# Performance work log

Hardware: AMD Instinct MI355X
Metric: run time of the kernel (lower is better)

The kernel has to match this reference:

```python
import jax, jax.numpy as jnp
import numpy as np

NUM_HEADS = 16


def rotate_half(x):
    x1 = x[..., ::2]
    x2 = x[..., 1::2]
    return jnp.concatenate((-x2, x1), axis=-1)


def rope_sin_cos(seq_len, head_dim, dtype):
    inv_freq = 1.0 / (10000.0 ** (jnp.arange(0, head_dim, 2, dtype=jnp.float32) / head_dim))
    t = jnp.arange(seq_len, dtype=jnp.float32)
    freqs = jnp.einsum('i,j->ij', t, inv_freq)          # [S, D/2]
    emb = jnp.concatenate((freqs, freqs), axis=-1)      # [S, D]
    return jnp.sin(emb).astype(dtype), jnp.cos(emb).astype(dtype)


def setup_inputs() -> dict:
    key = jax.random.key(0)
    B, S, E = 2, 2048, 2048
    ks = jax.random.split(key, 5)
    scale = 1.0 / np.sqrt(E)
    return {
        'x': jax.random.normal(ks[0], (B, S, E), dtype=jnp.float32),
        'mask': jnp.ones((B, S), dtype=jnp.int32),
        'Wq': jax.random.normal(ks[1], (E, E), dtype=jnp.float32) * scale,
        'bq': jnp.zeros((E,), dtype=jnp.float32),
        'Wk': jax.random.normal(ks[2], (E, E), dtype=jnp.float32) * scale,
        'bk': jnp.zeros((E,), dtype=jnp.float32),
        'Wv': jax.random.normal(ks[3], (E, E), dtype=jnp.float32) * scale,
        'bv': jnp.zeros((E,), dtype=jnp.float32),
        'Wo': jax.random.normal(ks[4], (E, E), dtype=jnp.float32) * scale,
        'bo': jnp.zeros((E,), dtype=jnp.float32),
    }


def reference(x, mask, Wq, bq, Wk, bk, Wv, bv, Wo, bo):
    B, S, E = x.shape
    H = NUM_HEADS
    D = E // H
    q = (x @ Wq + bq).reshape(B, S, H, D).transpose(0, 2, 1, 3)  # [B,H,S,D]
    k = (x @ Wk + bk).reshape(B, S, H, D).transpose(0, 2, 1, 3)
    v = (x @ Wv + bv).reshape(B, S, H, D).transpose(0, 2, 1, 3)

    sin, cos = rope_sin_cos(S, D, q.dtype)  # [S,D]
    sin = sin[None, None]                    # [1,1,S,D]
    cos = cos[None, None]
    q = q * cos + rotate_half(q) * sin
    k = k * cos + rotate_half(k) * sin

    scores = jnp.einsum('bhqd,bhkd->bhqk', q, k) / jnp.sqrt(jnp.asarray(D, q.dtype))
    scores = jnp.where(mask[:, None, None, :] == 0, -jnp.inf, scores)
    probs = jax.nn.softmax(scores, axis=-1)
    attn = jnp.einsum('bhqk,bhkd->bhqd', probs, v)       # [B,H,S,D]
    attn = attn.transpose(0, 2, 1, 3).reshape(B, S, E)
    return attn @ Wo + bo
```

## Files before the change

kernel.cpp:

```cpp
#include <hip/hip_runtime.h>
#include <hip/hip_bf16.h>
#include <cmath>

typedef unsigned short u16;
typedef unsigned int   u32;

using v4f    = __attribute__((ext_vector_type(4)))  float;
using f32x16 = __attribute__((ext_vector_type(16))) float;
using s8v    = __attribute__((ext_vector_type(8)))  short;
using u32x2  = __attribute__((ext_vector_type(2)))  unsigned int;

union Frag { uint4 u; s8v s; };

__device__ __forceinline__ u16 f2bf(float f){
  u32 u = __float_as_uint(f);
  u32 r = u + 0x7fffu + ((u >> 16) & 1u);
  return (u16)(r >> 16);
}
__device__ __forceinline__ float bf2f(u16 h){ return __uint_as_float(((u32)h) << 16); }

__device__ __forceinline__ u32 cvtpk(float a, float b){
  u32 r;
  asm("v_cvt_pk_bf16_f32 %0, %1, %2" : "=v"(r) : "v"(a), "v"(b));
  return r;
}

__device__ __forceinline__ void async16(const void* g, void* l){
  __builtin_amdgcn_global_load_lds((__attribute__((address_space(1))) void*)g,
                                   (__attribute__((address_space(3))) void*)l, 16, 0, 0);
}

__global__ __launch_bounds__(256) void prep_kernel(
    const float* __restrict__ x, u16* __restrict__ xb,
    const float* __restrict__ W0, const float* __restrict__ W1,
    const float* __restrict__ W2, const float* __restrict__ W3,
    u16* __restrict__ T0, u16* __restrict__ T1, u16* __restrict__ T2, u16* __restrict__ T3){
  __shared__ float tile[64][65];
  const int bid = blockIdx.x;
  if (bid < 8192){
    size_t i = ((size_t)bid * 256 + threadIdx.x) * 4;
    float4 v = *(const float4*)(x + i);
    uint2 o;
    o.x = (u32)f2bf(v.x) | ((u32)f2bf(v.y) << 16);
    o.y = (u32)f2bf(v.z) | ((u32)f2bf(v.w) << 16);
    *(uint2*)(xb + i) = o;
    return;
  }
  const int t4 = bid - 8192;
  const int z  = t4 >> 10;
  const float* W = (z==0)?W0:(z==1)?W1:(z==2)?W2:W3;
  u16*         T = (z==0)?T0:(z==1)?T1:(z==2)?T2:T3;
  const int k0 = ((t4 & 1023) >> 5)*64, n0 = (t4 & 31)*64;
  const int t  = threadIdx.x;
  const int rr = t >> 4, c4 = (t & 15) * 4;
  #pragma unroll
  for (int i=0;i<4;i++){
    int k = rr + i*16;
    float4 v = *(const float4*)(W + (size_t)(k0+k)*2048 + n0 + c4);
    tile[k][c4+0]=v.x; tile[k][c4+1]=v.y; tile[k][c4+2]=v.z; tile[k][c4+3]=v.w;
  }
  __syncthreads();
  #pragma unroll
  for (int i=0;i<4;i++){
    int n = rr + i*16;
    uint2 o;
    o.x = (u32)f2bf(tile[c4+0][n]) | ((u32)f2bf(tile[c4+1][n])<<16);
    o.y = (u32)f2bf(tile[c4+2][n]) | ((u32)f2bf(tile[c4+3][n])<<16);
    *(uint2*)(T + (size_t)(n0+n)*2048 + k0 + c4) = o;
  }
}

template<int MODE>
__device__ __forceinline__ void gemm_tile(const u16* __restrict__ A, const u16* __restrict__ BT,
                                          const float* __restrict__ bias, void* __restrict__ Cout,
                                          int m0, int n0, u16* sm){
  constexpr int K = 2048;
  u16* Asl = sm;
  u16* Bsl = sm + 8192;
  const int tid  = threadIdx.x;
  const int w    = tid >> 6;
  const int lane = tid & 63;
  const int r    = lane & 15, q = lane >> 4;
  const int wm   = (w >> 1) * 64, wn = (w & 1) * 64;

  v4f acc[4][4];
  #pragma unroll
  for (int i=0;i<4;i++)
    #pragma unroll
    for (int j=0;j<4;j++) acc[i][j] = (v4f)0.f;

  const int srow = w*32 + (lane>>3);
  const int sblk = (lane&7) ^ ((lane>>3)&7);
  const u16* Ag = A  + (size_t)(m0+srow)*K + sblk*8;
  const u16* Bg = BT + (size_t)(n0+srow)*K + sblk*8;
  u16* Als = Asl + (w*32)*64;
  u16* Bls = Bsl + (w*32)*64;

  for (int kk = 0; kk < K; kk += 64) {
    #pragma unroll
    for (int i=0;i<4;i++){
      async16(Ag + (size_t)i*8*K + kk, Als + i*512);
      async16(Bg + (size_t)i*8*K + kk, Bls + i*512);
    }
    __syncthreads();
    #pragma unroll
    for (int ks=0; ks<2; ++ks) {
      s8v af[4], bfr[4];
      #pragma unroll
      for (int i=0;i<4;i++){
        int rho = wm + i*16 + r;
        int p = (ks*4 + q) ^ (r&7);
        Frag t; t.u = *(const uint4*)(Asl + rho*64 + p*8); af[i] = t.s;
      }
      #pragma unroll
      for (int j=0;j<4;j++){
        int rho = wn + j*16 + r;
        int p = (ks*4 + q) ^ (r&7);
        Frag t; t.u = *(const uint4*)(Bsl + rho*64 + p*8); bfr[j] = t.s;
      }
      #pragma unroll
      for (int i=0;i<4;i++)
        #pragma unroll
        for (int j=0;j<4;j++)
          acc[i][j] = __builtin_amdgcn_mfma_f32_16x16x32_bf16(af[i], bfr[j], acc[i][j], 0, 0, 0);
    }
    __syncthreads();
  }

  float bv[4];
  #pragma unroll
  for (int j=0;j<4;j++) bv[j] = bias[n0 + wn + j*16 + r];

  if constexpr (MODE != 3){
    #pragma unroll
    for (int i=0;i<4;i++){
      #pragma unroll
      for (int j=0;j<4;j++){
        const int gn = n0 + wn + j*16 + r;
        #pragma unroll
        for (int rr2=0; rr2<4; ++rr2){
          const int gm = m0 + wm + i*16 + q*4 + rr2;
          float val = acc[i][j][rr2] + bv[j];
          if (MODE == 0) ((u16*)Cout)[(size_t)gm*2048 + gn] = f2bf(val);
          else           ((float*)Cout)[(size_t)gm*2048 + gn] = val;
        }
      }
    }
  } else {
    #pragma unroll
    for (int i=0;i<4;i++)
      #pragma unroll
      for (int j=0;j<4;j++){
        const int col = wn + j*16 + r;
        #pragma unroll
        for (int rr2=0; rr2<4; ++rr2)
          sm[(wm + i*16 + q*4 + rr2)*128 + col] = f2bf(acc[i][j][rr2] + bv[j]);
      }
    __syncthreads();
    const float invf = exp2f(-(float)lane * 0.20762050593045952f);
    for (int rr=0; rr<32; ++rr){
      const int row = w*32 + rr;
      const int s = (m0 + row) & 2047;
      float sn, cs;
      sincosf((float)s * invf, &sn, &cs);
      const u16* tr = sm + row*128;
      float x_j   = bf2f(tr[lane]);
      float x_j64 = bf2f(tr[64 + lane]);
      float x_2j  = bf2f(tr[2*lane]);
      float x_2j1 = bf2f(tr[2*lane + 1]);
      u16* gp = (u16*)Cout + (size_t)(m0 + row)*2048 + n0;
      gp[lane]      = f2bf(x_j  * cs - x_2j1 * sn);
      gp[64 + lane] = f2bf(x_j64 * cs + x_2j  * sn);
    }
  }
}

__global__ __launch_bounds__(256) void gemm_qkv_kernel(
    const u16* __restrict__ A,
    const u16* __restrict__ WqT, const u16* __restrict__ WkT, const u16* __restrict__ WvT,
    const float* __restrict__ bq, const float* __restrict__ bk, const float* __restrict__ bv,
    u16* __restrict__ Qb, u16* __restrict__ Kb, u16* __restrict__ Vb){
  __shared__ u16 sm[16384];
  const int bx = blockIdx.x, by = blockIdx.y;
  const int mat = bx >> 4;
  const u16*   BT   = (mat==0)?WqT:(mat==1)?WkT:WvT;
  const float* bias = (mat==0)?bq :(mat==1)?bk :bv;
  u16*         Cout = (mat==0)?Qb :(mat==1)?Kb :Vb;
  if (mat < 2) gemm_tile<3>(A, BT, bias, Cout, by*128, (bx & 15)*128, sm);
  else         gemm_tile<0>(A, BT, bias, Cout, by*128, (bx & 15)*128, sm);
}

__global__ __launch_bounds__(256) void gemm_wo_kernel(const u16* __restrict__ A,
                                                      const u16* __restrict__ WoT,
                                                      const float* __restrict__ bias,
                                                      float* __restrict__ out){
  __shared__ u16 sm[16384];
  gemm_tile<1>(A, WoT, bias, out, blockIdx.y*128, blockIdx.x*128, sm);
}

__global__ __launch_bounds__(256) void tv_kernel(const u16* __restrict__ V, u16* __restrict__ VT){
  __shared__ u16 t[64*72];
  const int tb = blockIdx.x;
  const int s0 = (tb & 31)*64;
  const int d0 = ((tb >> 5) & 1)*64;
  const int bh = tb >> 6;
  const int b = bh >> 4, h = bh & 15;
  const size_t obase = ((size_t)bh*128 + d0)*2048 + s0;
  const int tid = threadIdx.x;
  #pragma unroll
  for (int i=0;i<2;i++){
    int c = tid + i*256;
    int sl = c >> 3, dc = (c & 7) * 8;
    *(uint4*)(t + sl*72 + dc) =
      *(const uint4*)(V + ((size_t)(b*2048 + s0 + sl))*2048 + h*128 + d0 + dc);
  }
  __syncthreads();
  #pragma unroll
  for (int i=0;i<2;i++){
    int c = tid + i*256;
    int dl = c >> 3, sc4 = (c & 7) * 8;
    u16 tmp[8];
    #pragma unroll
    for (int j=0;j<8;j++) tmp[j] = t[(sc4+j)*72 + dl];
    *(uint4*)(VT + obase + (size_t)dl*2048 + sc4) = *(const uint4*)tmp;
  }
}

__global__ __launch_bounds__(256,2) void attn_kernel(const u16* __restrict__ Q,
                                                     const u16* __restrict__ K,
                                                     const u16* __restrict__ VT,
                                                     const int* __restrict__ mask,
                                                     u16* __restrict__ Out){
  constexpr int S = 2048;
  constexpr float SL2 = 0.08838834764831845f * 1.4426950408889634f;
  __shared__ u16 smem[32768];

  const int tid = threadIdx.x, w = tid >> 6, lane = tid & 63;
  const int qc = lane & 31;
  const int h  = lane >> 5;
  const int l7 = lane & 7;
  const int hh = blockIdx.y, b = blockIdx.z;
  const int q0 = blockIdx.x * 128;
  const size_t rowb = (size_t)b * 2048;
  const size_t bhD  = ((size_t)(b*16 + hh)) * 128;

  s8v qf[8];
  {
    const u16* qp = Q + (rowb + q0 + w*32 + qc)*2048 + hh*128 + h*8;
    #pragma unroll
    for (int t=0;t<8;t++){ Frag f; f.u = *(const uint4*)(qp + t*16); qf[t] = f.s; }
  }

  f32x16 accO[4];
  #pragma unroll
  for (int d=0; d<4; d++) accO[d] = (f32x16)0.f;
  float lsum = 0.f;

  const int sr4 = lane >> 4, sp16 = lane & 15;
  const int vr8 = lane >> 3, vp8 = lane & 7;

  auto stage = [&](u16* base, int key0){
    u16* Kd = base;
    u16* Vd = base + 8192;
    #pragma unroll
    for (int i=0;i<4;i++){
      int R = w*16 + i*4;
      int ob = sp16 ^ ((R&7) + sr4);
      async16(K + (rowb + key0 + R + sr4)*2048 + hh*128 + ob*8, Kd + R*128);
    }
    #pragma unroll
    for (int i=0;i<4;i++){
      int R = w*32 + i*8;
      int ob = vp8 ^ vr8;
      async16(VT + (bhD + R + vr8)*2048 + key0 + ob*8, Vd + R*64);
    }
  };

  stage(smem, 0);
  int mv = mask[b*S + lane];
  __syncthreads();
  unsigned long long bm = __ballot(mv != 0);
  int cur = 0;

  for (int it=0; it<32; ++it){
    if (it < 31){
      stage(smem + (cur^1)*16384, (it+1)*64);
      mv = mask[b*S + (it+1)*64 + lane];
    }
    const u16* Ks = smem + cur*16384;
    const u16* Vs = Ks + 8192;

    #pragma unroll
    for (int nb=0; nb<2; ++nb){
      f32x16 sc = (f32x16)0.f;
      __builtin_amdgcn_s_setprio(1);
      #pragma unroll
      for (int t=0;t<8;t++){
        Frag kf; kf.u = *(const uint4*)(Ks + (nb*32 + qc)*128 + (((2*t + h) ^ l7)*8));
        sc = __builtin_amdgcn_mfma_f32_32x32x16_bf16(kf.s, qf[t], sc, 0, 0, 0);
      }
      __builtin_amdgcn_s_setprio(0);
      float p[16];
      #pragma unroll
      for (int m=0; m<16; ++m) p[m] = exp2f(sc[m] * SL2);
      if (bm != ~0ull){
        #pragma unroll
        for (int m=0; m<16; ++m){
          int bit = nb*32 + (m&3) + 8*(m>>2) + 4*h;
          if (!((bm >> bit) & 1ull)) p[m] = 0.f;
        }
      }
      #pragma unroll
      for (int m=0; m<16; ++m) lsum += p[m];

      #pragma unroll
      for (int g=0; g<2; ++g){
        u32 a0 = cvtpk(p[8*g+0], p[8*g+1]);
        u32 a1 = cvtpk(p[8*g+2], p[8*g+3]);
        u32 a2 = cvtpk(p[8*g+4], p[8*g+5]);
        u32 a3 = cvtpk(p[8*g+6], p[8*g+7]);
        u32x2 r0 = __builtin_amdgcn_permlane32_swap(a0, a2, false, false);
        u32x2 r1 = __builtin_amdgcn_permlane32_swap(a1, a3, false, false);
        Frag pf; pf.u = make_uint4(r0[0], r1[0], r0[1], r1[1]);
        const int T = nb*2 + g;
        __builtin_amdgcn_s_setprio(1);
        #pragma unroll
        for (int d=0; d<4; ++d){
          Frag vf; vf.u = *(const uint4*)(Vs + (d*32 + qc)*64 + (((2*T + h) ^ l7)*8));
          accO[d] = __builtin_amdgcn_mfma_f32_32x32x16_bf16(vf.s, pf.s, accO[d], 0, 0, 0);
        }
        __builtin_amdgcn_s_setprio(0);
      }
    }
    __syncthreads();
    bm = __ballot(mv != 0);
    cur ^= 1;
  }

  float sall = lsum + __shfl_xor(lsum, 32, 64);
  float invv = (sall > 0.f) ? 1.f/sall : 0.f;
  u16* orow = Out + (rowb + q0 + w*32 + qc)*2048 + hh*128;
  #pragma unroll
  for (int d=0; d<4; ++d){
    #pragma unroll
    for (int g2=0; g2<4; ++g2){
      uint2 o;
      o.x = cvtpk(accO[d][g2*4+0] * invv, accO[d][g2*4+1] * invv);
      o.y = cvtpk(accO[d][g2*4+2] * invv, accO[d][g2*4+3] * invv);
      *(uint2*)(orow + d*32 + g2*8 + 4*h) = o;
    }
  }
}

extern "C" void kernel_launch(void* const* d_in, const int* in_sizes, int n_in,
                              void* d_out, int out_size, void* d_ws, size_t ws_size,
                              hipStream_t stream) {
  (void)in_sizes; (void)n_in; (void)out_size; (void)ws_size;
  const float* x    = (const float*)d_in[0];
  const int*   mask = (const int*)d_in[1];
  const float* Wq   = (const float*)d_in[2];
  const float* bq   = (const float*)d_in[3];
  const float* Wk   = (const float*)d_in[4];
  const float* bk   = (const float*)d_in[5];
  const float* Wv   = (const float*)d_in[6];
  const float* bv   = (const float*)d_in[7];
  const float* Wo   = (const float*)d_in[8];
  const float* bo   = (const float*)d_in[9];

  u16* xbf = (u16*)d_ws;
  u16* WqT = xbf + 8388608;
  u16* WkT = WqT + 4194304;
  u16* WvT = WkT + 4194304;
  u16* WoT = WvT + 4194304;
  u16* Qb  = WoT + 4194304;
  u16* Kb  = Qb + 8388608;
  u16* Vb  = Kb + 8388608;
  u16* VTb = Vb + 8388608;
  u16* Ab  = VTb + 8388608;

  prep_kernel<<<12288, 256, 0, stream>>>(x, xbf, Wq, Wk, Wv, Wo, WqT, WkT, WvT, WoT);
  gemm_qkv_kernel<<<dim3(48,32), 256, 0, stream>>>(xbf, WqT, WkT, WvT, bq, bk, bv, Qb, Kb, Vb);
  tv_kernel<<<2048, 256, 0, stream>>>(Vb, VTb);
  attn_kernel<<<dim3(16,16,2), 256, 0, stream>>>(Qb, Kb, VTb, mask, Ab);
  gemm_wo_kernel<<<dim3(16,32), 256, 0, stream>>>(Ab, WoT, bo, (float*)d_out);
}
```

Before: 404.3 us.

## Precompute RoPE sin/cos table and shrink attention blocks with single-buffered staging

The prep kernel gains extra blocks that build a sin/cos table, stored in the attention-output buffer, and the QKV GEMM RoPE epilogue reads it instead of calling sincosf per element. The attention kernel now uses 2 waves (64 query rows) per block, twice as many blocks, and a single LDS buffer with no prefetch, halving shared memory per block to allow more resident blocks. In exchange, K/V loads no longer overlap compute within a block, and the loads are issued by fewer threads.

After: 421.8 us. 1.04x slower.

```diff
diff --git a/kernel.cpp b/kernel.cpp
--- a/kernel.cpp
+++ b/kernel.cpp
@@ -34,7 +34,8 @@
     const float* __restrict__ x, u16* __restrict__ xb,
     const float* __restrict__ W0, const float* __restrict__ W1,
     const float* __restrict__ W2, const float* __restrict__ W3,
-    u16* __restrict__ T0, u16* __restrict__ T1, u16* __restrict__ T2, u16* __restrict__ T3){
+    u16* __restrict__ T0, u16* __restrict__ T1, u16* __restrict__ T2, u16* __restrict__ T3,
+    float2* __restrict__ tab){
   __shared__ float tile[64][65];
   const int bid = blockIdx.x;
   if (bid < 8192){
@@ -46,6 +47,15 @@
     *(uint2*)(xb + i) = o;
     return;
   }
+  if (bid >= 12288){
+    const int idx = (bid - 12288)*256 + threadIdx.x;
+    const int s = idx >> 6, j = idx & 63;
+    float invf = exp2f(-(float)j * 0.20762050593045952f);
+    float sn, cs;
+    sincosf((float)s * invf, &sn, &cs);
+    tab[idx] = make_float2(sn, cs);
+    return;
+  }
   const int t4 = bid - 8192;
   const int z  = t4 >> 10;
   const float* W = (z==0)?W0:(z==1)?W1:(z==2)?W2:W3;
@@ -73,7 +83,7 @@
 template<int MODE>
 __device__ __forceinline__ void gemm_tile(const u16* __restrict__ A, const u16* __restrict__ BT,
                                           const float* __restrict__ bias, void* __restrict__ Cout,
-                                          int m0, int n0, u16* sm){
+                                          int m0, int n0, u16* sm, const float2* __restrict__ tab){
   constexpr int K = 2048;
   u16* Asl = sm;
   u16* Bsl = sm + 8192;
@@ -157,20 +167,18 @@
           sm[(wm + i*16 + q*4 + rr2)*128 + col] = f2bf(acc[i][j][rr2] + bv[j]);
       }
     __syncthreads();
-    const float invf = exp2f(-(float)lane * 0.20762050593045952f);
     for (int rr=0; rr<32; ++rr){
       const int row = w*32 + rr;
       const int s = (m0 + row) & 2047;
-      float sn, cs;
-      sincosf((float)s * invf, &sn, &cs);
+      float2 sc2 = tab[s*64 + lane];
       const u16* tr = sm + row*128;
       float x_j   = bf2f(tr[lane]);
       float x_j64 = bf2f(tr[64 + lane]);
       float x_2j  = bf2f(tr[2*lane]);
       float x_2j1 = bf2f(tr[2*lane + 1]);
       u16* gp = (u16*)Cout + (size_t)(m0 + row)*2048 + n0;
-      gp[lane]      = f2bf(x_j  * cs - x_2j1 * sn);
-      gp[64 + lane] = f2bf(x_j64 * cs + x_2j  * sn);
+      gp[lane]      = f2bf(x_j  * sc2.y - x_2j1 * sc2.x);
+      gp[64 + lane] = f2bf(x_j64 * sc2.y + x_2j  * sc2.x);
     }
   }
 }
@@ -179,15 +187,16 @@
     const u16* __restrict__ A,
     const u16* __restrict__ WqT, const u16* __restrict__ WkT, const u16* __restrict__ WvT,
     const float* __restrict__ bq, const float* __restrict__ bk, const float* __restrict__ bv,
-    u16* __restrict__ Qb, u16* __restrict__ Kb, u16* __restrict__ Vb){
+    u16* __restrict__ Qb, u16* __restrict__ Kb, u16* __restrict__ Vb,
+    const float2* __restrict__ tab){
   __shared__ u16 sm[16384];
   const int bx = blockIdx.x, by = blockIdx.y;
   const int mat = bx >> 4;
   const u16*   BT   = (mat==0)?WqT:(mat==1)?WkT:WvT;
   const float* bias = (mat==0)?bq :(mat==1)?bk :bv;
   u16*         Cout = (mat==0)?Qb :(mat==1)?Kb :Vb;
-  if (mat < 2) gemm_tile<3>(A, BT, bias, Cout, by*128, (bx & 15)*128, sm);
-  else         gemm_tile<0>(A, BT, bias, Cout, by*128, (bx & 15)*128, sm);
+  if (mat < 2) gemm_tile<3>(A, BT, bias, Cout, by*128, (bx & 15)*128, sm, tab);
+  else         gemm_tile<0>(A, BT, bias, Cout, by*128, (bx & 15)*128, sm, tab);
 }
 
 __global__ __launch_bounds__(256) void gemm_wo_kernel(const u16* __restrict__ A,
@@ -195,7 +204,7 @@
                                                       const float* __restrict__ bias,
                                                       float* __restrict__ out){
   __shared__ u16 sm[16384];
-  gemm_tile<1>(A, WoT, bias, out, blockIdx.y*128, blockIdx.x*128, sm);
+  gemm_tile<1>(A, WoT, bias, out, blockIdx.y*128, blockIdx.x*128, sm, nullptr);
 }
 
 __global__ __launch_bounds__(256) void tv_kernel(const u16* __restrict__ V, u16* __restrict__ VT){
@@ -226,21 +235,21 @@
   }
 }
 
-__global__ __launch_bounds__(256,2) void attn_kernel(const u16* __restrict__ Q,
+__global__ __launch_bounds__(128,2) void attn_kernel(const u16* __restrict__ Q,
                                                      const u16* __restrict__ K,
                                                      const u16* __restrict__ VT,
                                                      const int* __restrict__ mask,
                                                      u16* __restrict__ Out){
   constexpr int S = 2048;
   constexpr float SL2 = 0.08838834764831845f * 1.4426950408889634f;
-  __shared__ u16 smem[32768];
+  __shared__ u16 smem[16384];
 
   const int tid = threadIdx.x, w = tid >> 6, lane = tid & 63;
   const int qc = lane & 31;
   const int h  = lane >> 5;
   const int l7 = lane & 7;
   const int hh = blockIdx.y, b = blockIdx.z;
-  const int q0 = blockIdx.x * 128;
+  const int q0 = blockIdx.x * 64;
   const size_t rowb = (size_t)b * 2048;
   const size_t bhD  = ((size_t)(b*16 + hh)) * 128;
 
@@ -259,36 +268,25 @@
   const int sr4 = lane >> 4, sp16 = lane & 15;
   const int vr8 = lane >> 3, vp8 = lane & 7;
 
-  auto stage = [&](u16* base, int key0){
-    u16* Kd = base;
-    u16* Vd = base + 8192;
-    #pragma unroll
-    for (int i=0;i<4;i++){
-      int R = w*16 + i*4;
+  for (int it=0; it<32; ++it){
+    const int key0 = it*64;
+    int mv = mask[b*S + key0 + lane];
+    #pragma unroll
+    for (int i=0;i<8;i++){
+      int R = w*32 + i*4;
       int ob = sp16 ^ ((R&7) + sr4);
-      async16(K + (rowb + key0 + R + sr4)*2048 + hh*128 + ob*8, Kd + R*128);
-    }
-    #pragma unroll
-    for (int i=0;i<4;i++){
-      int R = w*32 + i*8;
+      async16(K + (rowb + key0 + R + sr4)*2048 + hh*128 + ob*8, smem + R*128);
+    }
+    #pragma unroll
+    for (int i=0;i<8;i++){
+      int R = w*64 + i*8;
       int ob = vp8 ^ vr8;
-      async16(VT + (bhD + R + vr8)*2048 + key0 + ob*8, Vd + R*64);
-    }
-  };
-
-  stage(smem, 0);
-  int mv = mask[b*S + lane];
-  __syncthreads();
-  unsigned long long bm = __ballot(mv != 0);
-  int cur = 0;
-
-  for (int it=0; it<32; ++it){
-    if (it < 31){
-      stage(smem + (cur^1)*16384, (it+1)*64);
-      mv = mask[b*S + (it+1)*64 + lane];
-    }
-    const u16* Ks = smem + cur*16384;
-    const u16* Vs = Ks + 8192;
+      async16(VT + (bhD + R + vr8)*2048 + key0 + ob*8, smem + 8192 + R*64);
+    }
+    __syncthreads();
+    unsigned long long bm = __ballot(mv != 0);
+    const u16* Ks = smem;
+    const u16* Vs = smem + 8192;
 
     #pragma unroll
     for (int nb=0; nb<2; ++nb){
@@ -333,8 +331,6 @@
       }
     }
     __syncthreads();
-    bm = __ballot(mv != 0);
-    cur ^= 1;
   }
 
   float sall = lsum + __shfl_xor(lsum, 32, 64);
@@ -377,10 +373,11 @@
   u16* Vb  = Kb + 8388608;
   u16* VTb = Vb + 8388608;
   u16* Ab  = VTb + 8388608;
-
-  prep_kernel<<<12288, 256, 0, stream>>>(x, xbf, Wq, Wk, Wv, Wo, WqT, WkT, WvT, WoT);
-  gemm_qkv_kernel<<<dim3(48,32), 256, 0, stream>>>(xbf, WqT, WkT, WvT, bq, bk, bv, Qb, Kb, Vb);
+  float2* tab = (float2*)Ab;
+
+  prep_kernel<<<12800, 256, 0, stream>>>(x, xbf, Wq, Wk, Wv, Wo, WqT, WkT, WvT, WoT, tab);
+  gemm_qkv_kernel<<<dim3(48,32), 256, 0, stream>>>(xbf, WqT, WkT, WvT, bq, bk, bv, Qb, Kb, Vb, tab);
   tv_kernel<<<2048, 256, 0, stream>>>(Vb, VTb);
-  attn_kernel<<<dim3(16,16,2), 256, 0, stream>>>(Qb, Kb, VTb, mask, Ab);
+  attn_kernel<<<dim3(32,16,2), 128, 0, stream>>>(Qb, Kb, VTb, mask, Ab);
   gemm_wo_kernel<<<dim3(16,32), 256, 0, stream>>>(Ab, WoT, bo, (float*)d_out);
 }
```
